# Kernel optimization log

Hardware: AMD Instinct MI355X
Metric: run time of the kernel (lower is better)

Reference implementation:

```python
import jax, jax.numpy as jnp
import numpy as np

N_NODES = 100000
N_EDGES = 1600000
NUM_GRAPHS = 128
EPS = 1e-5


def _glorot(key, shape):
    fan_in, fan_out = shape
    lim = np.sqrt(6.0 / (fan_in + fan_out))
    return jax.random.uniform(key, shape, jnp.float32, -lim, lim)


def setup_inputs() -> dict:
    key = jax.random.key(0)
    ks = jax.random.split(key, 24)
    inp = {
        "x": jax.random.normal(ks[0], (N_NODES, 32), jnp.float32),
        "edge_index": jax.random.randint(ks[1], (2, N_EDGES), 0, N_NODES, jnp.int32),
        "batch": jnp.sort(jax.random.randint(ks[2], (N_NODES,), 0, NUM_GRAPHS, jnp.int32)),
        # SAGEConv params: Wl acts on mean-aggregated neighbors (with bias), Wr on root (no bias)
        "w1_l": _glorot(ks[3], (32, 16)), "b1": jnp.zeros((16,), jnp.float32), "w1_r": _glorot(ks[4], (32, 16)),
        "w2_l": _glorot(ks[5], (16, 64)), "b2": jnp.zeros((64,), jnp.float32), "w2_r": _glorot(ks[6], (16, 64)),
        "w3_l": _glorot(ks[7], (64, 512)), "b3": jnp.zeros((512,), jnp.float32), "w3_r": _glorot(ks[8], (64, 512)),
        # BatchNorm params
        "g1": jnp.ones((16,), jnp.float32), "be1": jnp.zeros((16,), jnp.float32),
        "g2": jnp.ones((64,), jnp.float32), "be2": jnp.zeros((64,), jnp.float32),
        "g3": jnp.ones((512,), jnp.float32), "be3": jnp.zeros((512,), jnp.float32),
        # MLP head
        "w_l1": _glorot(ks[9], (512, 256)), "b_l1": jnp.zeros((256,), jnp.float32),
        "w_l2": _glorot(ks[10], (256, 10)), "b_l2": jnp.zeros((10,), jnp.float32),
    }
    return inp


def _sage_conv(x, src, dst, w_l, b_l, w_r):
    # mean-aggregate neighbor features (messages flow src -> dst)
    msg = x[src]                                              # [E, d_in]
    s = jax.ops.segment_sum(msg, dst, num_segments=N_NODES)   # [N, d_in]
    cnt = jax.ops.segment_sum(jnp.ones((src.shape[0],), x.dtype), dst, num_segments=N_NODES)
    mean = s / jnp.maximum(cnt, 1.0)[:, None]
    return mean @ w_l + b_l + x @ w_r


def _bn(x, g, b):
    m = jnp.mean(x, axis=0)
    v = jnp.var(x, axis=0)  # biased, as torch BN training-mode normalization
    return (x - m) * jax.lax.rsqrt(v + EPS) * g + b


def reference(x, edge_index, batch,
              w1_l, b1, w1_r, w2_l, b2, w2_r, w3_l, b3, w3_r,
              g1, be1, g2, be2, g3, be3,
              w_l1, b_l1, w_l2, b_l2):
    src, dst = edge_index[0], edge_index[1]
    h = _sage_conv(x, src, dst, w1_l, b1, w1_r)
    h = jax.nn.relu(_bn(h, g1, be1))
    h = _sage_conv(h, src, dst, w2_l, b2, w2_r)
    h = jax.nn.relu(_bn(h, g2, be2))
    # dropout (p=0.25) treated as identity (eval mode)
    h = _sage_conv(h, src, dst, w3_l, b3, w3_r)
    h = jax.nn.relu(_bn(h, g3, be3))
    # global max pooling per graph
    pooled = jax.ops.segment_max(h, batch, num_segments=NUM_GRAPHS)  # [G, 512]
    out = jax.nn.relu(pooled @ w_l1 + b_l1)
    # dropout (p=0.5) treated as identity (eval mode)
    return out @ w_l2 + b_l2
```

## Files before the change

### kernel.cpp

```cpp
#include <hip/hip_runtime.h>
#include <hip/hip_bf16.h>
#include <cstdint>

#define NUM_GRAPHS 128
constexpr float EPSF = 1e-5f;

using short8 = __attribute__((ext_vector_type(8))) short;
using f32x4  = __attribute__((ext_vector_type(4))) float;

__device__ __forceinline__ unsigned int enc_key(float f) {
  unsigned int b = __float_as_uint(f);
  return (b & 0x80000000u) ? ~b : (b | 0x80000000u);
}
__device__ __forceinline__ float dec_key(unsigned int k) {
  return __uint_as_float((k & 0x80000000u) ? (k ^ 0x80000000u) : ~k);
}

__device__ __forceinline__ unsigned int f2bf(float v) {
  unsigned int u = __float_as_uint(v);
  u += 0x7FFFu + ((u >> 16) & 1u);
  return (u >> 16) & 0xFFFFu;
}
__device__ __forceinline__ float bf2f(unsigned int h) {
  return __uint_as_float(h << 16);
}

__device__ __forceinline__ size_t aswz(int n, int kunit) {
  return ((size_t)(n >> 4) * 8 + kunit) * 128 + (size_t)(n & 15) * 8;
}

__device__ __forceinline__ float4 bnrelu4(float4 v, const float4 A, const float4 B) {
  v.x = fmaxf(fmaf(v.x, A.x, B.x), 0.f);
  v.y = fmaxf(fmaf(v.y, A.y, B.y), 0.f);
  v.z = fmaxf(fmaf(v.z, A.z, B.z), 0.f);
  v.w = fmaxf(fmaf(v.w, A.w, B.w), 0.f);
  return v;
}


__global__ __launch_bounds__(256) void bhist_kernel(const int* __restrict__ dst,
                                                    int* __restrict__ bcnt, int E) {
  __shared__ int hist[256];
  const int t = threadIdx.x;
  const int e0 = blockIdx.x * 8192;
  const int e1 = min(e0 + 8192, E);
  hist[t] = 0;
  __syncthreads();
  for (int e = e0 + t; e < e1; e += 256) atomicAdd(&hist[dst[e] >> 9], 1);
  __syncthreads();
  if (hist[t]) atomicAdd(&bcnt[t], hist[t]);
}

__global__ void bscan_kernel(const int* __restrict__ bcnt, int* __restrict__ bbase,
                             int* __restrict__ bcur, int E) {
  __shared__ int ts[256];
  const int t = threadIdx.x;
  int v = bcnt[t];
  ts[t] = v;
  __syncthreads();
  for (int off = 1; off < 256; off <<= 1) {
    int add = (t >= off) ? ts[t - off] : 0;
    __syncthreads();
    ts[t] += add;
    __syncthreads();
  }
  int excl = ts[t] - v;
  bbase[t] = excl;
  bcur[t] = excl;
  if (t == 255) bbase[256] = E;
}

__global__ __launch_bounds__(256) void bucketA_kernel(const int* __restrict__ src,
                                                      const int* __restrict__ dst,
                                                      int* __restrict__ bcur,
                                                      unsigned int* __restrict__ ebuf, int E) {
  __shared__ int hist[256];
  __shared__ int base[256];
  const int t = threadIdx.x;
  const int e0 = blockIdx.x * 8192;
  const int e1 = min(e0 + 8192, E);
  hist[t] = 0;
  __syncthreads();
  for (int e = e0 + t; e < e1; e += 256) atomicAdd(&hist[dst[e] >> 9], 1);
  __syncthreads();
  int c = hist[t];
  base[t] = c ? atomicAdd(&bcur[t], c) : 0;
  hist[t] = 0;
  __syncthreads();
  for (int e = e0 + t; e < e1; e += 256) {
    int d = dst[e];
    int b = d >> 9;
    int p = base[b] + atomicAdd(&hist[b], 1);
    ebuf[p] = (unsigned int)src[e] | ((unsigned int)(d & 511) << 23);
  }
}

__global__ __launch_bounds__(256) void bucketCSR_kernel(
    const unsigned int* __restrict__ ebufp, const int* __restrict__ bbase,
    int* __restrict__ rowptr, int* __restrict__ csr, int N, int E) {
  __shared__ unsigned int eb[12288];
  __shared__ int hist[512];
  __shared__ int ts[256];
  const int b = blockIdx.x;
  const int t = threadIdx.x;
  const int lo = bbase[b], hi = bbase[b + 1];
  const int cnt = hi - lo;
  const bool stage = (cnt <= 12288);
  hist[t] = 0;
  hist[t + 256] = 0;
  __syncthreads();
  if (stage) {
    for (int i = t; i < cnt; i += 256) {
      unsigned int e = ebufp[lo + i];
      eb[i] = e;
      atomicAdd(&hist[e >> 23], 1);
    }
  } else {
    for (int i = t; i < cnt; i += 256) atomicAdd(&hist[ebufp[lo + i] >> 23], 1);
  }
  __syncthreads();
  const int h0 = hist[2 * t], h1 = hist[2 * t + 1];
  const int psum = h0 + h1;
  ts[t] = psum;
  __syncthreads();
  for (int off = 1; off < 256; off <<= 1) {
    int add = (t >= off) ? ts[t - off] : 0;
    __syncthreads();
    ts[t] += add;
    __syncthreads();
  }
  const int pexcl = ts[t] - psum;
  hist[2 * t] = lo + pexcl;
  hist[2 * t + 1] = lo + pexcl + h0;
  __syncthreads();
  const int nbase = b << 9;
  if (nbase + 2 * t < N) rowptr[nbase + 2 * t] = hist[2 * t];
  if (nbase + 2 * t + 1 < N) rowptr[nbase + 2 * t + 1] = hist[2 * t + 1];
  if (b == 0 && t == 0) rowptr[N] = E;
  __syncthreads();
  if (stage) {
    for (int i = t; i < cnt; i += 256) {
      unsigned int e = eb[i];
      int pos = atomicAdd(&hist[e >> 23], 1);
      csr[pos] = (int)(e & 0x7FFFFFu);
    }
  } else {
    for (int i = t; i < cnt; i += 256) {
      unsigned int e = ebufp[lo + i];
      int pos = atomicAdd(&hist[e >> 23], 1);
      csr[pos] = (int)(e & 0x7FFFFFu);
    }
  }
}

__global__ __launch_bounds__(256) void pool_init_kernel(unsigned int* __restrict__ pmax,
                                                        unsigned int* __restrict__ pmin, int n) {
  int i = blockIdx.x * 256 + threadIdx.x;
  if (i < n) { pmax[i] = 0x007FFFFFu; pmin[i] = 0xFF800000u; }
}

__global__ __launch_bounds__(256) void proj1_kernel(const float* __restrict__ x,
                                                    const float* __restrict__ wl,
                                                    float* __restrict__ t1, int N) {
  __shared__ float w[32 * 16];
  const int t = threadIdx.x;
  if (t < 128) reinterpret_cast<float4*>(w)[t] = reinterpret_cast<const float4*>(wl)[t];
  __syncthreads();
  const int n = blockIdx.x * 256 + t;
  if (n >= N) return;
  float xr[32];
  const float4* xp = reinterpret_cast<const float4*>(x + (size_t)n * 32);
#pragma unroll
  for (int i = 0; i < 8; ++i) {
    float4 v = xp[i];
    xr[4 * i] = v.x; xr[4 * i + 1] = v.y; xr[4 * i + 2] = v.z; xr[4 * i + 3] = v.w;
  }
  float o[16];
#pragma unroll
  for (int j = 0; j < 16; ++j) o[j] = 0.f;
#pragma unroll
  for (int k = 0; k < 32; ++k) {
    float xv = xr[k];
#pragma unroll
    for (int j = 0; j < 16; ++j) o[j] = fmaf(xv, w[k * 16 + j], o[j]);
  }
  float4* op = reinterpret_cast<float4*>(t1 + (size_t)n * 16);
#pragma unroll
  for (int i = 0; i < 4; ++i) op[i] = make_float4(o[4 * i], o[4 * i + 1], o[4 * i + 2], o[4 * i + 3]);
}

__global__ __launch_bounds__(256) void linear1_kernel(
    const int* __restrict__ rowptr, const int* __restrict__ csr,
    const float* __restrict__ t1, const float* __restrict__ x,
    const float* __restrict__ bias, const float* __restrict__ wr,
    float* __restrict__ out, float* __restrict__ bnsum_out, int N) {
  constexpr int K2P = 49;
  __shared__ float As[64 * K2P];
  const int nb = blockIdx.x * 64;
  const int tid = threadIdx.x;

  {
    const int nl = tid >> 2, t = tid & 3;
    const int n = nb + nl;
    float4 acc = make_float4(0.f, 0.f, 0.f, 0.f);
    float sc = 0.f;
    if (n < N) {
      const int r0 = rowptr[n], r1 = rowptr[n + 1];
      int p = r0;
      for (; p + 8 <= r1; p += 8) {
        int s[8];
#pragma unroll
        for (int u = 0; u < 8; ++u) s[u] = csr[p + u];
        float4 v[8];
#pragma unroll
        for (int u = 0; u < 8; ++u)
          v[u] = reinterpret_cast<const float4*>(t1 + (size_t)s[u] * 16)[t];
#pragma unroll
        for (int u = 0; u < 8; ++u) {
          acc.x += v[u].x; acc.y += v[u].y; acc.z += v[u].z; acc.w += v[u].w;
        }
      }
      for (; p < r1; ++p) {
        float4 v = reinterpret_cast<const float4*>(t1 + (size_t)csr[p] * 16)[t];
        acc.x += v.x; acc.y += v.y; acc.z += v.z; acc.w += v.w;
      }
      sc = 1.0f / fmaxf((float)(r1 - r0), 1.0f);
    }
    As[nl * K2P + t * 4 + 0] = acc.x * sc;
    As[nl * K2P + t * 4 + 1] = acc.y * sc;
    As[nl * K2P + t * 4 + 2] = acc.z * sc;
    As[nl * K2P + t * 4 + 3] = acc.w * sc;
  }

  {
    for (int idx4 = tid; idx4 < 64 * 8; idx4 += 256) {
      int nl = idx4 >> 3, k4 = idx4 & 7;
      int n = nb + nl;
      float4 v = make_float4(0.f, 0.f, 0.f, 0.f);
      if (n < N) v = reinterpret_cast<const float4*>(x + (size_t)n * 32)[k4];
      As[nl * K2P + 16 + k4 * 4 + 0] = v.x;
      As[nl * K2P + 16 + k4 * 4 + 1] = v.y;
      As[nl * K2P + 16 + k4 * 4 + 2] = v.z;
      As[nl * K2P + 16 + k4 * 4 + 3] = v.w;
    }
  }
  __syncthreads();

  const int ty = tid >> 4, tx = tid & 15;
  float acc[4] = {0.f, 0.f, 0.f, 0.f};
  const float* A0 = &As[(ty * 4 + 0) * K2P + 16];
  const float* A1 = &As[(ty * 4 + 1) * K2P + 16];
  const float* A2 = &As[(ty * 4 + 2) * K2P + 16];
  const float* A3 = &As[(ty * 4 + 3) * K2P + 16];
#pragma unroll 4
  for (int k = 0; k < 32; ++k) {
    float w = wr[(size_t)k * 16 + tx];
    acc[0] = fmaf(A0[k], w, acc[0]);
    acc[1] = fmaf(A1[k], w, acc[1]);
    acc[2] = fmaf(A2[k], w, acc[2]);
    acc[3] = fmaf(A3[k], w, acc[3]);
  }

  const float bv = bias[tx];
  float s = 0.f, q = 0.f;
#pragma unroll
  for (int r = 0; r < 4; ++r) {
    int n = nb + ty * 4 + r;
    if (n < N) {
      float v = acc[r] + As[(ty * 4 + r) * K2P + tx] + bv;
      out[(size_t)n * 16 + tx] = v;
      s += v;
      q += v * v;
    }
  }

  __syncthreads();
  float* sL = As;
  float* qL = As + 16 * 16;
  sL[ty * 16 + tx] = s;
  qL[ty * 16 + tx] = q;
  __syncthreads();
  float* bn = bnsum_out + (size_t)(blockIdx.x & 7) * 32;
  if (tid < 16) {
    float ss = 0.f, qq = 0.f;
#pragma unroll
    for (int t = 0; t < 16; ++t) { ss += sL[t * 16 + tid]; qq += qL[t * 16 + tid]; }
    atomicAdd(&bn[tid], ss);
    atomicAdd(&bn[16 + tid], qq);
  }
}

template <int D, int R>
__global__ void bn_finalizeR(const float* __restrict__ sums, const float* __restrict__ g,
                             const float* __restrict__ be, float* __restrict__ ab, float invN) {
  int f = blockIdx.x * blockDim.x + threadIdx.x;
  if (f >= D) return;
  float m = 0.f, q = 0.f;
#pragma unroll
  for (int r = 0; r < R; ++r) {
    m += sums[r * 2 * D + f];
    q += sums[r * 2 * D + D + f];
  }
  m *= invN;
  float var = q * invN - m * m;
  float a = g[f] * rsqrtf(var + EPSF);
  ab[f] = a;
  ab[D + f] = be[f] - m * a;
}

__global__ __launch_bounds__(256) void prep2_kernel(const float* __restrict__ h1,
                                                    const float* __restrict__ ab,
                                                    unsigned short* __restrict__ h1b, int N) {
  int n = blockIdx.x * 256 + threadIdx.x;
  if (n >= N) return;
  const float4* hp = reinterpret_cast<const float4*>(h1 + (size_t)n * 16);
  unsigned int o[8];
#pragma unroll
  for (int i = 0; i < 4; ++i) {
    float4 v = hp[i];
    const float4 A = *reinterpret_cast<const float4*>(&ab[i * 4]);
    const float4 B = *reinterpret_cast<const float4*>(&ab[16 + i * 4]);
    v = bnrelu4(v, A, B);
    o[2 * i] = f2bf(v.x) | (f2bf(v.y) << 16);
    o[2 * i + 1] = f2bf(v.z) | (f2bf(v.w) << 16);
  }
  uint4* op = reinterpret_cast<uint4*>(h1b + (size_t)n * 16);
  op[0] = make_uint4(o[0], o[1], o[2], o[3]);
  op[1] = make_uint4(o[4], o[5], o[6], o[7]);
}

__global__ __launch_bounds__(256) void linear2b_kernel(
    const int* __restrict__ rowptr, const int* __restrict__ csr,
    const unsigned short* __restrict__ h1b, const float* __restrict__ wl,
    const float* __restrict__ bias, const float* __restrict__ wr,
    float* __restrict__ out, float* __restrict__ bnsum_out, int N) {
  constexpr int K2P = 33;
  __shared__ float As[64 * K2P];
  const int nb = blockIdx.x * 64;
  const int tid = threadIdx.x;

  {
    const int nl = tid >> 2, t = tid & 3;
    const int n = nb + nl;
    float4 acc = make_float4(0.f, 0.f, 0.f, 0.f);
    float sc = 0.f;
    if (n < N) {
      const int r0 = rowptr[n], r1 = rowptr[n + 1];
      int p = r0;
      for (; p + 8 <= r1; p += 8) {
        int s[8];
#pragma unroll
        for (int u = 0; u < 8; ++u) s[u] = csr[p + u];
        uint2 v[8];
#pragma unroll
        for (int u = 0; u < 8; ++u)
          v[u] = *reinterpret_cast<const uint2*>(h1b + (size_t)s[u] * 16 + t * 4);
#pragma unroll
        for (int u = 0; u < 8; ++u) {
          acc.x += bf2f(v[u].x & 0xFFFFu);
          acc.y += bf2f(v[u].x >> 16);
          acc.z += bf2f(v[u].y & 0xFFFFu);
          acc.w += bf2f(v[u].y >> 16);
        }
      }
      for (; p < r1; ++p) {
        uint2 v = *reinterpret_cast<const uint2*>(h1b + (size_t)csr[p] * 16 + t * 4);
        acc.x += bf2f(v.x & 0xFFFFu);
        acc.y += bf2f(v.x >> 16);
        acc.z += bf2f(v.y & 0xFFFFu);
        acc.w += bf2f(v.y >> 16);
      }
      sc = 1.0f / fmaxf((float)(r1 - r0), 1.0f);
    }
    As[nl * K2P + t * 4 + 0] = acc.x * sc;
    As[nl * K2P + t * 4 + 1] = acc.y * sc;
    As[nl * K2P + t * 4 + 2] = acc.z * sc;
    As[nl * K2P + t * 4 + 3] = acc.w * sc;
  }

  if (tid < 128) {
    int nl = tid >> 1, half = tid & 1;
    int n = nb + nl;
    uint4 u = make_uint4(0, 0, 0, 0);
    if (n < N) u = *reinterpret_cast<const uint4*>(h1b + (size_t)n * 16 + half * 8);
    float* d = &As[nl * K2P + 16 + half * 8];
    d[0] = bf2f(u.x & 0xFFFFu); d[1] = bf2f(u.x >> 16);
    d[2] = bf2f(u.y & 0xFFFFu); d[3] = bf2f(u.y >> 16);
    d[4] = bf2f(u.z & 0xFFFFu); d[5] = bf2f(u.z >> 16);
    d[6] = bf2f(u.w & 0xFFFFu); d[7] = bf2f(u.w >> 16);
  }
  __syncthreads();

  const int ty = tid >> 4, tx = tid & 15;
  const int j0 = tx * 4;
  float acc[4][4];
#pragma unroll
  for (int r = 0; r < 4; ++r)
#pragma unroll
    for (int c = 0; c < 4; ++c) acc[r][c] = 0.f;

  const float* A0 = &As[(ty * 4 + 0) * K2P];
  const float* A1 = &As[(ty * 4 + 1) * K2P];
  const float* A2 = &As[(ty * 4 + 2) * K2P];
  const float* A3 = &As[(ty * 4 + 3) * K2P];

#pragma unroll 4
  for (int k = 0; k < 16; ++k) {
    const float4 w = *reinterpret_cast<const float4*>(wl + (size_t)k * 64 + j0);
    const float wv[4] = {w.x, w.y, w.z, w.w};
    float a0 = A0[k], a1 = A1[k], a2 = A2[k], a3 = A3[k];
#pragma unroll
    for (int c = 0; c < 4; ++c) {
      acc[0][c] = fmaf(a0, wv[c], acc[0][c]);
      acc[1][c] = fmaf(a1, wv[c], acc[1][c]);
      acc[2][c] = fmaf(a2, wv[c], acc[2][c]);
      acc[3][c] = fmaf(a3, wv[c], acc[3][c]);
    }
  }
#pragma unroll 4
  for (int k = 0; k < 16; ++k) {
    const float4 w = *reinterpret_cast<const float4*>(wr + (size_t)k * 64 + j0);
    const float wv[4] = {w.x, w.y, w.z, w.w};
    float a0 = A0[16 + k], a1 = A1[16 + k], a2 = A2[16 + k], a3 = A3[16 + k];
#pragma unroll
    for (int c = 0; c < 4; ++c) {
      acc[0][c] = fmaf(a0, wv[c], acc[0][c]);
      acc[1][c] = fmaf(a1, wv[c], acc[1][c]);
      acc[2][c] = fmaf(a2, wv[c], acc[2][c]);
      acc[3][c] = fmaf(a3, wv[c], acc[3][c]);
    }
  }

  float bv[4];
#pragma unroll
  for (int c = 0; c < 4; ++c) bv[c] = bias[j0 + c];

  float s[4], q[4];
#pragma unroll
  for (int c = 0; c < 4; ++c) { s[c] = 0.f; q[c] = 0.f; }
#pragma unroll
  for (int r = 0; r < 4; ++r) {
    int n = nb + ty * 4 + r;
    if (n < N) {
#pragma unroll
      for (int c = 0; c < 4; ++c) {
        float v = acc[r][c] + bv[c];
        out[(size_t)n * 64 + j0 + c] = v;
        s[c] += v;
        q[c] += v * v;
      }
    }
  }

  __syncthreads();
  float* sL = As;
  float* qL = As + 16 * 64;
#pragma unroll
  for (int c = 0; c < 4; ++c) {
    sL[ty * 64 + tx * 4 + c] = s[c];
    qL[ty * 64 + tx * 4 + c] = q[c];
  }
  __syncthreads();
  float* bn = bnsum_out + (size_t)(blockIdx.x & 7) * 128;
  for (int f = tid; f < 64; f += 256) {
    float ss = 0.f, qq = 0.f;
#pragma unroll
    for (int t = 0; t < 16; ++t) { ss += sL[t * 64 + f]; qq += qL[t * 64 + f]; }
    atomicAdd(&bn[f], ss);
    atomicAdd(&bn[64 + f], qq);
  }
}

__global__ __launch_bounds__(256) void prep3_kernel(const float* __restrict__ h2,
                                                    const float* __restrict__ ab,
                                                    unsigned short* __restrict__ xh,
                                                    unsigned short* __restrict__ xlin,
                                                    int N) {
  const int t = threadIdx.x;
  const int rg = t >> 7, ku = (t >> 4) & 7, r = t & 15;
  const int n = blockIdx.x * 32 + rg * 16 + r;
  if (n >= N) return;
  const float* hp = h2 + (size_t)n * 64 + ku * 8;
  const float4 v0 = *reinterpret_cast<const float4*>(hp);
  const float4 v1 = *reinterpret_cast<const float4*>(hp + 4);
  const float4 A0 = *reinterpret_cast<const float4*>(&ab[ku * 8]);
  const float4 A1 = *reinterpret_cast<const float4*>(&ab[ku * 8 + 4]);
  const float4 B0 = *reinterpret_cast<const float4*>(&ab[64 + ku * 8]);
  const float4 B1 = *reinterpret_cast<const float4*>(&ab[64 + ku * 8 + 4]);
  float rr[8];
  rr[0] = fmaxf(fmaf(v0.x, A0.x, B0.x), 0.f);
  rr[1] = fmaxf(fmaf(v0.y, A0.y, B0.y), 0.f);
  rr[2] = fmaxf(fmaf(v0.z, A0.z, B0.z), 0.f);
  rr[3] = fmaxf(fmaf(v0.w, A0.w, B0.w), 0.f);
  rr[4] = fmaxf(fmaf(v1.x, A1.x, B1.x), 0.f);
  rr[5] = fmaxf(fmaf(v1.y, A1.y, B1.y), 0.f);
  rr[6] = fmaxf(fmaf(v1.z, A1.z, B1.z), 0.f);
  rr[7] = fmaxf(fmaf(v1.w, A1.w, B1.w), 0.f);
  unsigned int uh[4];
#pragma unroll
  for (int j = 0; j < 4; ++j)
    uh[j] = f2bf(rr[2 * j]) | (f2bf(rr[2 * j + 1]) << 16);
  const size_t off = aswz(n, ku);
  *reinterpret_cast<uint4*>(xh + off) = make_uint4(uh[0], uh[1], uh[2], uh[3]);
  *reinterpret_cast<uint4*>(xlin + (size_t)n * 64 + ku * 8) =
      make_uint4(uh[0], uh[1], uh[2], uh[3]);
}

__global__ __launch_bounds__(256) void convw3_kernel(const float* __restrict__ wl,
                                                     const float* __restrict__ wr,
                                                     unsigned short* __restrict__ bth) {
  int idx = blockIdx.x * 256 + threadIdx.x;
  if (idx >= 512 * 16) return;
  const int c = idx >> 4, ku = idx & 15;
  unsigned int uh[4];
#pragma unroll
  for (int jj = 0; jj < 4; ++jj) {
    unsigned int hh[2];
#pragma unroll
    for (int t = 0; t < 2; ++t) {
      int k = ku * 8 + jj * 2 + t;
      float w = (k < 64) ? wl[(size_t)k * 512 + c] : wr[(size_t)(k - 64) * 512 + c];
      hh[t] = f2bf(w);
    }
    uh[jj] = hh[0] | (hh[1] << 16);
  }
  const size_t off = ((size_t)(c >> 4) * 16 + ku) * 128 + (size_t)(c & 15) * 8;
  *reinterpret_cast<uint4*>(bth + off) = make_uint4(uh[0], uh[1], uh[2], uh[3]);
}

__global__ __launch_bounds__(256) void gather_mean_bf16(
    const unsigned short* __restrict__ xlin, const int* __restrict__ rowptr,
    const int* __restrict__ csr, unsigned short* __restrict__ mh, int N) {
  const int t = threadIdx.x;
  const int n = blockIdx.x * 32 + (t >> 3);
  const int ku = t & 7;
  if (n >= N) return;
  float acc[8];
#pragma unroll
  for (int i = 0; i < 8; ++i) acc[i] = 0.f;
  const int r0 = rowptr[n], r1 = rowptr[n + 1];
  int p = r0;
  for (; p + 8 <= r1; p += 8) {
    int s[8];
#pragma unroll
    for (int u = 0; u < 8; ++u) s[u] = csr[p + u];
    uint4 u4[8];
#pragma unroll
    for (int u = 0; u < 8; ++u)
      u4[u] = *reinterpret_cast<const uint4*>(xlin + (size_t)s[u] * 64 + ku * 8);
#pragma unroll
    for (int u = 0; u < 8; ++u) {
      const unsigned int uu[4] = {u4[u].x, u4[u].y, u4[u].z, u4[u].w};
#pragma unroll
      for (int j = 0; j < 4; ++j) {
        acc[2 * j]     += bf2f(uu[j] & 0xFFFFu);
        acc[2 * j + 1] += bf2f(uu[j] >> 16);
      }
    }
  }
  for (; p < r1; ++p) {
    const int s = csr[p];
    const uint4 u = *reinterpret_cast<const uint4*>(xlin + (size_t)s * 64 + ku * 8);
    const unsigned int uu[4] = {u.x, u.y, u.z, u.w};
#pragma unroll
    for (int j = 0; j < 4; ++j) {
      acc[2 * j]     += bf2f(uu[j] & 0xFFFFu);
      acc[2 * j + 1] += bf2f(uu[j] >> 16);
    }
  }
  const float sc = 1.0f / fmaxf((float)(r1 - r0), 1.0f);
  unsigned int oh[4];
#pragma unroll
  for (int j = 0; j < 4; ++j)
    oh[j] = f2bf(acc[2 * j] * sc) | (f2bf(acc[2 * j + 1] * sc) << 16);
  const size_t off = aswz(n, ku);
  *reinterpret_cast<uint4*>(mh + off) = make_uint4(oh[0], oh[1], oh[2], oh[3]);
}

__global__ __launch_bounds__(256) void mfma3_kernel(
    const unsigned short* __restrict__ mh, const unsigned short* __restrict__ xh,
    const unsigned short* __restrict__ bth, const float* __restrict__ bias,
    const int* __restrict__ batchp, float* __restrict__ bnsum,
    unsigned int* __restrict__ pmax, unsigned int* __restrict__ pmin, int N) {
  __shared__ int gb[64];
  const int tid = threadIdx.x;
  const int nb = blockIdx.x * 64;
  const int colbase = blockIdx.y * 256;
  if (tid < 64) gb[tid] = (nb + tid < N) ? batchp[nb + tid] : 0x7FFFFFFF;
  __syncthreads();

  const int wid = tid >> 6, lane = tid & 63;
  const int l16 = lane & 15, lg = lane >> 4;
  const int wcol = colbase + wid * 64;
  const int rgb = blockIdx.x * 4;

  f32x4 acc[4][4];
#pragma unroll
  for (int rb = 0; rb < 4; ++rb)
#pragma unroll
    for (int cb = 0; cb < 4; ++cb) acc[rb][cb] = (f32x4){0.f, 0.f, 0.f, 0.f};

  const int abase = rgb * 1024 + lg * 128 + l16 * 8;
  const int bbase = (wcol >> 4) * 2048 + lg * 128 + l16 * 8;

#pragma unroll
  for (int ks = 0; ks < 4; ++ks) {
    const unsigned short* APh = (ks < 2) ? mh : xh;
    const int aoff = abase + (ks & 1) * 512;
    short8 ah[4];
#pragma unroll
    for (int rb = 0; rb < 4; ++rb)
      ah[rb] = *reinterpret_cast<const short8*>(APh + aoff + rb * 1024);
#pragma unroll
    for (int cb = 0; cb < 4; ++cb) {
      const short8 bh = *reinterpret_cast<const short8*>(bth + bbase + cb * 2048 + ks * 512);
#pragma unroll
      for (int rb = 0; rb < 4; ++rb) {
        acc[rb][cb] = __builtin_amdgcn_mfma_f32_16x16x32_bf16(ah[rb], bh, acc[rb][cb], 0, 0, 0);
      }
    }
  }

  float* bn = bnsum + (size_t)(blockIdx.x & 7) * 1024;
  const bool uni = (gb[0] == gb[63]);
  const bool full = (nb + 64 <= N);
  const int g0 = gb[0];

  if (full) {
#pragma unroll
    for (int cb = 0; cb < 4; ++cb) {
      const int col = wcol + cb * 16 + l16;
      const float bv = bias[col];
      float s0 = 0.f, q0 = 0.f, mx0 = -INFINITY, mn0 = INFINITY;
#pragma unroll
      for (int rb = 0; rb < 4; ++rb)
#pragma unroll
        for (int r = 0; r < 4; ++r) {
          const float a = acc[rb][cb][r];
          s0 += a;
          q0 = fmaf(a, a, q0);
          mx0 = fmaxf(mx0, a);
          mn0 = fminf(mn0, a);
        }
      s0 += __shfl_xor(s0, 16); s0 += __shfl_xor(s0, 32);
      q0 += __shfl_xor(q0, 16); q0 += __shfl_xor(q0, 32);
      if (lane < 16) {
        atomicAdd(&bn[col], fmaf(64.f, bv, s0));
        atomicAdd(&bn[512 + col], q0 + 2.f * bv * s0 + 64.f * bv * bv);
      }
      if (uni) {
        mx0 = fmaxf(mx0, __shfl_xor(mx0, 16)); mx0 = fmaxf(mx0, __shfl_xor(mx0, 32));
        mn0 = fminf(mn0, __shfl_xor(mn0, 16)); mn0 = fminf(mn0, __shfl_xor(mn0, 32));
        if (lane < 16) {
          atomicMax(&pmax[(size_t)g0 * 512 + col], enc_key(mx0 + bv));
          atomicMin(&pmin[(size_t)g0 * 512 + col], enc_key(mn0 + bv));
        }
      } else {
        int curg = -1;
        float rmx = -INFINITY, rmn = INFINITY;
#pragma unroll
        for (int rb = 0; rb < 4; ++rb)
#pragma unroll
          for (int r = 0; r < 4; ++r) {
            const int row = rb * 16 + lg * 4 + r;
            const int g = gb[row];
            if (g != curg) {
              if (curg >= 0) {
                atomicMax(&pmax[(size_t)curg * 512 + col], enc_key(rmx + bv));
                atomicMin(&pmin[(size_t)curg * 512 + col], enc_key(rmn + bv));
              }
              curg = g; rmx = -INFINITY; rmn = INFINITY;
            }
            const float a = acc[rb][cb][r];
            rmx = fmaxf(rmx, a); rmn = fminf(rmn, a);
          }
        if (curg >= 0) {
          atomicMax(&pmax[(size_t)curg * 512 + col], enc_key(rmx + bv));
          atomicMin(&pmin[(size_t)curg * 512 + col], enc_key(rmn + bv));
        }
      }
    }
  } else {
#pragma unroll
    for (int cb = 0; cb < 4; ++cb) {
      const int col = wcol + cb * 16 + l16;
      const float bv = bias[col];
      float s = 0.f, q = 0.f;
#pragma unroll
      for (int rb = 0; rb < 4; ++rb)
#pragma unroll
        for (int r = 0; r < 4; ++r) {
          const int row = rb * 16 + lg * 4 + r;
          float v = acc[rb][cb][r] + bv;
          acc[rb][cb][r] = v;
          if (nb + row < N) {
            s += v; q += v * v;
          }
        }
      s += __shfl_xor(s, 16); s += __shfl_xor(s, 32);
      q += __shfl_xor(q, 16); q += __shfl_xor(q, 32);
      if (lane < 16) {
        atomicAdd(&bn[col], s);
        atomicAdd(&bn[512 + col], q);
      }
      int curg = -1;
      float rmx = -INFINITY, rmn = INFINITY;
#pragma unroll
      for (int rb = 0; rb < 4; ++rb)
#pragma unroll
        for (int r = 0; r < 4; ++r) {
          const int row = rb * 16 + lg * 4 + r;
          const int g = gb[row];
          if (g != curg) {
            if (curg >= 0 && curg != 0x7FFFFFFF) {
              atomicMax(&pmax[(size_t)curg * 512 + col], enc_key(rmx));
              atomicMin(&pmin[(size_t)curg * 512 + col], enc_key(rmn));
            }
            curg = g; rmx = -INFINITY; rmn = INFINITY;
          }
          if (g != 0x7FFFFFFF) {
            const float v = acc[rb][cb][r];
            rmx = fmaxf(rmx, v); rmn = fminf(rmn, v);
          }
        }
      if (curg >= 0 && curg != 0x7FFFFFFF) {
        atomicMax(&pmax[(size_t)curg * 512 + col], enc_key(rmx));
        atomicMin(&pmin[(size_t)curg * 512 + col], enc_key(rmn));
      }
    }
  }
}

__global__ __launch_bounds__(256) void head_kernel(const unsigned int* __restrict__ pmax,
                                                   const unsigned int* __restrict__ pmin,
                                                   const float* __restrict__ ab,
                                                   const float* __restrict__ w1,
                                                   const float* __restrict__ b1,
                                                   const float* __restrict__ w2,
                                                   const float* __restrict__ b2,
                                                   float* __restrict__ out) {
  __shared__ float pr[512];
  __shared__ float hid[256];
  int g = blockIdx.x;
  int t = threadIdx.x;
  for (int i = t; i < 512; i += 256) {
    float a = ab[i], b = ab[512 + i];
    float v = (a >= 0.f) ? dec_key(pmax[(size_t)g * 512 + i])
                         : dec_key(pmin[(size_t)g * 512 + i]);
    pr[i] = fmaxf(fmaf(v, a, b), 0.f);
  }
  __syncthreads();
  float acc = b1[t];
  for (int i = 0; i < 512; ++i) acc = fmaf(pr[i], w1[(size_t)i * 256 + t], acc);
  hid[t] = fmaxf(acc, 0.f);
  __syncthreads();
  if (t < 10) {
    float o = b2[t];
    for (int j = 0; j < 256; ++j) o = fmaf(hid[j], w2[(size_t)j * 10 + t], o);
    out[(size_t)g * 10 + t] = o;
  }
}

extern "C" void kernel_launch(void* const* d_in, const int* in_sizes, int n_in,
                              void* d_out, int out_size, void* d_ws, size_t ws_size,
                              hipStream_t stream) {
  const float* x    = (const float*)d_in[0];
  const int*   ei   = (const int*)d_in[1];
  const int*   batch= (const int*)d_in[2];
  const float* w1_l = (const float*)d_in[3];
  const float* b1   = (const float*)d_in[4];
  const float* w1_r = (const float*)d_in[5];
  const float* w2_l = (const float*)d_in[6];
  const float* b2   = (const float*)d_in[7];
  const float* w2_r = (const float*)d_in[8];
  const float* w3_l = (const float*)d_in[9];
  const float* b3   = (const float*)d_in[10];
  const float* w3_r = (const float*)d_in[11];
  const float* g1   = (const float*)d_in[12];
  const float* be1  = (const float*)d_in[13];
  const float* g2   = (const float*)d_in[14];
  const float* be2  = (const float*)d_in[15];
  const float* g3   = (const float*)d_in[16];
  const float* be3  = (const float*)d_in[17];
  const float* wl1  = (const float*)d_in[18];
  const float* bl1  = (const float*)d_in[19];
  const float* wl2  = (const float*)d_in[20];
  const float* bl2  = (const float*)d_in[21];

  const int N = in_sizes[0] / 32;
  const int E = in_sizes[1] / 2;
  const int* src  = ei;
  const int* dstp = ei + E;
  float* outp = (float*)d_out;

  const int gx3 = (N + 63) / 64;
  const int Npad = gx3 * 64;
  const int nbuck = (N + 511) >> 9;

  size_t off = 0;
  auto alloc = [&](size_t bytes) -> void* {
    void* p = (char*)d_ws + off;
    off += (bytes + 255) & ~(size_t)255;
    return p;
  };
  int*   rowptr = (int*)alloc(((size_t)N + 1) * 4);
  int*   csr    = (int*)alloc((size_t)E * 4);
  int*   bcnt   = (int*)alloc(256 * 4);
  int*   bbase  = (int*)alloc(257 * 4);
  int*   bcur   = (int*)alloc(256 * 4);
  unsigned int* ebuf = (unsigned int*)alloc((size_t)E * 4);
  float* t1     = (float*)alloc((size_t)N * 16 * 4);
  float* h1     = (float*)alloc((size_t)N * 16 * 4);
  unsigned short* h1b = (unsigned short*)alloc((size_t)N * 16 * 2);
  float* h2     = (float*)alloc((size_t)N * 64 * 4);
  unsigned short* xh = (unsigned short*)alloc((size_t)Npad * 64 * 2);
  unsigned short* mh = (unsigned short*)alloc((size_t)Npad * 64 * 2);
  unsigned short* xlin = (unsigned short*)alloc((size_t)N * 64 * 2);
  unsigned short* bth = (unsigned short*)alloc(512 * 128 * 2);
  float* bnsum1 = (float*)alloc(8 * 32 * 4);
  float* bnsum2 = (float*)alloc(8 * 128 * 4);
  float* bnsum3 = (float*)alloc(8 * 1024 * 4);
  float* bnab1  = (float*)alloc(2 * 16 * 4);
  float* bnab2  = (float*)alloc(2 * 64 * 4);
  float* bnab3  = (float*)alloc(2 * 512 * 4);
  unsigned int* pmax = (unsigned int*)alloc((size_t)NUM_GRAPHS * 512 * 4);
  unsigned int* pmin = (unsigned int*)alloc((size_t)NUM_GRAPHS * 512 * 4);
  (void)ws_size;

  const float invN = 1.0f / (float)N;

  hipMemsetAsync(bcnt, 0, 256 * 4, stream);
  bhist_kernel<<<(E + 8191) / 8192, 256, 0, stream>>>(dstp, bcnt, E);
  bscan_kernel<<<1, 256, 0, stream>>>(bcnt, bbase, bcur, E);
  bucketA_kernel<<<(E + 8191) / 8192, 256, 0, stream>>>(src, dstp, bcur, ebuf, E);
  bucketCSR_kernel<<<nbuck, 256, 0, stream>>>(ebuf, bbase, rowptr, csr, N, E);

  pool_init_kernel<<<(NUM_GRAPHS * 512 + 255) / 256, 256, 0, stream>>>(
      pmax, pmin, NUM_GRAPHS * 512);
  convw3_kernel<<<(512 * 16 + 255) / 256, 256, 0, stream>>>(w3_l, w3_r, bth);

  if (Npad > N && (N & 15) == 0) {
    const size_t padBytes = (size_t)(Npad - N) * 64 * 2;
    hipMemsetAsync(xh + (size_t)N * 64, 0, padBytes, stream);
    hipMemsetAsync(mh + (size_t)N * 64, 0, padBytes, stream);
  }

  hipMemsetAsync(bnsum1, 0, 8 * 32 * 4, stream);
  proj1_kernel<<<(N + 255) / 256, 256, 0, stream>>>(x, w1_l, t1, N);
  linear1_kernel<<<(N + 63) / 64, 256, 0, stream>>>(
      rowptr, csr, t1, x, b1, w1_r, h1, bnsum1, N);
  bn_finalizeR<16, 8><<<1, 16, 0, stream>>>(bnsum1, g1, be1, bnab1, invN);

  prep2_kernel<<<(N + 255) / 256, 256, 0, stream>>>(h1, bnab1, h1b, N);
  hipMemsetAsync(bnsum2, 0, 8 * 128 * 4, stream);
  linear2b_kernel<<<(N + 63) / 64, 256, 0, stream>>>(
      rowptr, csr, h1b, w2_l, b2, w2_r, h2, bnsum2, N);
  bn_finalizeR<64, 8><<<1, 64, 0, stream>>>(bnsum2, g2, be2, bnab2, invN);

  prep3_kernel<<<(N + 31) / 32, 256, 0, stream>>>(h2, bnab2, xh, xlin, N);
  gather_mean_bf16<<<(N + 31) / 32, 256, 0, stream>>>(xlin, rowptr, csr, mh, N);
  hipMemsetAsync(bnsum3, 0, 8 * 1024 * 4, stream);
  mfma3_kernel<<<dim3(gx3, 2), 256, 0, stream>>>(
      mh, xh, bth, b3, batch, bnsum3, pmax, pmin, N);
  bn_finalizeR<512, 8><<<1, 512, 0, stream>>>(bnsum3, g3, be3, bnab3, invN);

  head_kernel<<<NUM_GRAPHS, 256, 0, stream>>>(pmax, pmin, bnab3, wl1, bl1, wl2, bl2, outp);
}
```

Measured before the change: 255.5 us.

## Merge mfma3 column blocks into one 512-thread block with double-buffered operand loads

The layer-3 MFMA kernel now launches one 512-thread block per 64-row tile covering all 512 output columns, instead of two 256-thread blocks each covering 256 columns. The per-tile batch-id load and the A-operand reads are shared across more waves. The K loop is software-pipelined with two register buffers, so loads for the next K step are issued before the current step's MFMAs, and s_setprio raises wave priority around the MFMA bursts. This is meant to hide global-load latency and halve redundant setup work, at the cost of higher register pressure and fewer, larger blocks.

Result: no change. 259.7 us (+1.6%).

```diff
diff --git a/kernel.cpp b/kernel.cpp
--- a/kernel.cpp
+++ b/kernel.cpp
@@ -577,7 +577,7 @@
   *reinterpret_cast<uint4*>(mh + off) = make_uint4(oh[0], oh[1], oh[2], oh[3]);
 }
 
-__global__ __launch_bounds__(256) void mfma3_kernel(
+__global__ __launch_bounds__(512) void mfma3_kernel(
     const unsigned short* __restrict__ mh, const unsigned short* __restrict__ xh,
     const unsigned short* __restrict__ bth, const float* __restrict__ bias,
     const int* __restrict__ batchp, float* __restrict__ bnsum,
@@ -585,13 +585,12 @@
   __shared__ int gb[64];
   const int tid = threadIdx.x;
   const int nb = blockIdx.x * 64;
-  const int colbase = blockIdx.y * 256;
   if (tid < 64) gb[tid] = (nb + tid < N) ? batchp[nb + tid] : 0x7FFFFFFF;
   __syncthreads();
 
   const int wid = tid >> 6, lane = tid & 63;
   const int l16 = lane & 15, lg = lane >> 4;
-  const int wcol = colbase + wid * 64;
+  const int wcol = wid * 64;
   const int rgb = blockIdx.x * 4;
 
   f32x4 acc[4][4];
@@ -603,22 +602,50 @@
   const int abase = rgb * 1024 + lg * 128 + l16 * 8;
   const int bbase = (wcol >> 4) * 2048 + lg * 128 + l16 * 8;
 
+  short8 ahA[4], bhA[4], ahB[4], bhB[4];
+#pragma unroll
+  for (int rb = 0; rb < 4; ++rb)
+    ahA[rb] = *reinterpret_cast<const short8*>(mh + abase + rb * 1024);
+#pragma unroll
+  for (int cb = 0; cb < 4; ++cb)
+    bhA[cb] = *reinterpret_cast<const short8*>(bth + bbase + cb * 2048);
+
 #pragma unroll
   for (int ks = 0; ks < 4; ++ks) {
-    const unsigned short* APh = (ks < 2) ? mh : xh;
-    const int aoff = abase + (ks & 1) * 512;
-    short8 ah[4];
-#pragma unroll
-    for (int rb = 0; rb < 4; ++rb)
-      ah[rb] = *reinterpret_cast<const short8*>(APh + aoff + rb * 1024);
-#pragma unroll
-    for (int cb = 0; cb < 4; ++cb) {
-      const short8 bh = *reinterpret_cast<const short8*>(bth + bbase + cb * 2048 + ks * 512);
-#pragma unroll
-      for (int rb = 0; rb < 4; ++rb) {
-        acc[rb][cb] = __builtin_amdgcn_mfma_f32_16x16x32_bf16(ah[rb], bh, acc[rb][cb], 0, 0, 0);
-      }
-    }
+    if (ks < 3) {
+      const unsigned short* APn = ((ks + 1) < 2) ? mh : xh;
+      const int naoff = abase + ((ks + 1) & 1) * 512;
+      if ((ks & 1) == 0) {
+#pragma unroll
+        for (int rb = 0; rb < 4; ++rb)
+          ahB[rb] = *reinterpret_cast<const short8*>(APn + naoff + rb * 1024);
+#pragma unroll
+        for (int cb = 0; cb < 4; ++cb)
+          bhB[cb] = *reinterpret_cast<const short8*>(bth + bbase + cb * 2048 + (ks + 1) * 512);
+      } else {
+#pragma unroll
+        for (int rb = 0; rb < 4; ++rb)
+          ahA[rb] = *reinterpret_cast<const short8*>(APn + naoff + rb * 1024);
+#pragma unroll
+        for (int cb = 0; cb < 4; ++cb)
+          bhA[cb] = *reinterpret_cast<const short8*>(bth + bbase + cb * 2048 + (ks + 1) * 512);
+      }
+    }
+    __builtin_amdgcn_s_setprio(1);
+    if ((ks & 1) == 0) {
+#pragma unroll
+      for (int cb = 0; cb < 4; ++cb)
+#pragma unroll
+        for (int rb = 0; rb < 4; ++rb)
+          acc[rb][cb] = __builtin_amdgcn_mfma_f32_16x16x32_bf16(ahA[rb], bhA[cb], acc[rb][cb], 0, 0, 0);
+    } else {
+#pragma unroll
+      for (int cb = 0; cb < 4; ++cb)
+#pragma unroll
+        for (int rb = 0; rb < 4; ++rb)
+          acc[rb][cb] = __builtin_amdgcn_mfma_f32_16x16x32_bf16(ahB[rb], bhB[cb], acc[rb][cb], 0, 0, 0);
+    }
+    __builtin_amdgcn_s_setprio(0);
   }
 
   float* bn = bnsum + (size_t)(blockIdx.x & 7) * 1024;
@@ -860,7 +887,7 @@
   prep3_kernel<<<(N + 31) / 32, 256, 0, stream>>>(h2, bnab2, xh, xlin, N);
   gather_mean_bf16<<<(N + 31) / 32, 256, 0, stream>>>(xlin, rowptr, csr, mh, N);
   hipMemsetAsync(bnsum3, 0, 8 * 1024 * 4, stream);
-  mfma3_kernel<<<dim3(gx3, 2), 256, 0, stream>>>(
+  mfma3_kernel<<<gx3, 512, 0, stream>>>(
       mh, xh, bth, b3, batch, bnsum3, pmax, pmin, N);
   bn_finalizeR<512, 8><<<1, 512, 0, stream>>>(bnsum3, g3, be3, bnab3, invN);
 
```
